# Kernel tuning notes

Hardware: AMD Instinct MI355X
Metric: run time of the kernel (lower is better)

The kernel has to match this reference:

```python
import jax, jax.numpy as jnp
import numpy as np


def setup_inputs() -> dict:
    key = jax.random.key(0)
    ks = jax.random.split(key, 8)
    B, T, C = 8, 2048, 1024
    X = jax.random.normal(ks[0], (B, T, C), dtype=jnp.float32)
    dX = jax.random.normal(ks[1], (B, T, C), dtype=jnp.float32)
    S_n = jnp.zeros((B, C), dtype=jnp.float32)
    att_mask = jnp.ones((B, T), dtype=jnp.int64)
    # parameters (torch init: randn(C,C)/C ; nn.Linear default uniform)
    W_Q = jax.random.normal(ks[2], (C, C), dtype=jnp.float32) / C
    W_K = jax.random.normal(ks[3], (C, C), dtype=jnp.float32) / C
    W_V = jax.random.normal(ks[4], (C, C), dtype=jnp.float32) / C
    bound = 1.0 / np.sqrt(C)
    W_hh = jax.random.uniform(ks[5], (C, C), minval=-bound, maxval=bound, dtype=jnp.float32)
    b_hh = jax.random.uniform(ks[6], (C,), minval=-bound, maxval=bound, dtype=jnp.float32)
    return {"X": X, "dX": dX, "S_n": S_n, "att_mask": att_mask,
            "W_Q": W_Q, "W_K": W_K, "W_V": W_V, "W_hh": W_hh, "b_hh": b_hh}


def reference(X, dX, S_n, att_mask, W_Q, W_K, W_V, W_hh, b_hh):
    B, T, C = X.shape
    # chunk_len is hard-coded to 1 in the source, so per-step:
    #   Q_t,K_t,V_t: [B,1,C]; c_t = Q_t @ K_t^T: [B,1,1]; A_t = c_t @ V_t.
    # These have no cross-timestep dependency -> precompute in parallel.
    Q = jax.nn.relu(jnp.einsum('btc,cd->btd', X, W_Q))
    K = jax.nn.relu(jnp.einsum('btc,cd->btd', X, W_K))
    V = jnp.einsum('btc,cd->btd', X, W_V)
    s = jnp.sum(Q * K, axis=-1, keepdims=True)        # [B,T,1]
    A = s * V                                          # [B,T,C]
    # A_factor = A_scale[chunk_len-1] = linspace(0,-1,ceil(T/2))[0] == 0.0
    A_scale = jnp.concatenate([jnp.linspace(0.0, -1.0, (T + 1) // 2),
                               jnp.linspace(-1.0, 0.0, T // 2)])
    A_factor = A_scale[0]

    def step(carry, A_t):
        h, prev_A = carry
        h_new = jnp.tanh(h @ W_hh.T + b_hh + A_t + prev_A * A_factor)
        return (h_new, A_t), h_new

    h0 = jnp.zeros((B, C), X.dtype)
    A_seq = jnp.swapaxes(A, 0, 1)                      # [T,B,C]
    _, H = jax.lax.scan(step, (h0, h0), A_seq)
    out = jnp.swapaxes(H, 0, 1)                        # [B,T,C]
    return out, S_n
```

## Files before the change

### kernel.cpp

```cpp
#include <hip/hip_runtime.h>
#include <hip/hip_bf16.h>

#define Bn 8
#define Tn 2048
#define Cn 1024

typedef __attribute__((ext_vector_type(8))) short short8;
typedef __attribute__((ext_vector_type(4))) float f32x4;

__device__ __forceinline__ unsigned short f2bf(float x) {
    union { float f; unsigned u; } v; v.f = x;
    return (unsigned short)((v.u + 0x7FFFu + ((v.u >> 16) & 1u)) >> 16);
}

__global__ __launch_bounds__(256) void transpose_cvt(const float* __restrict__ W,
                                                     unsigned short* __restrict__ WT) {
    __shared__ float tile[64][65];
    const int bx = blockIdx.x;
    const int tr = (bx >> 4) << 6;
    const int tc = (bx & 15) << 6;
    const int tid = threadIdx.x;
    const int r  = tid >> 2;
    const int c4 = (tid & 3) << 4;
#pragma unroll
    for (int i = 0; i < 4; ++i) {
        float4 v = *(const float4*)(W + (long)(tr + r) * Cn + tc + c4 + i * 4);
        tile[r][c4 + i * 4 + 0] = v.x;
        tile[r][c4 + i * 4 + 1] = v.y;
        tile[r][c4 + i * 4 + 2] = v.z;
        tile[r][c4 + i * 4 + 3] = v.w;
    }
    __syncthreads();
    short8 p0, p1;
#pragma unroll
    for (int i = 0; i < 8; ++i)  p0[i] = (short)f2bf(tile[c4 + i][r]);
#pragma unroll
    for (int i = 0; i < 8; ++i)  p1[i] = (short)f2bf(tile[c4 + 8 + i][r]);
    unsigned short* dst = WT + (long)(tc + r) * Cn + tr + c4;
    *(short8*)(dst)     = p0;
    *(short8*)(dst + 8) = p1;
}

__global__ __launch_bounds__(256, 1) void qkv_fused(const float* __restrict__ X,
                                                    const unsigned short* __restrict__ WqT,
                                                    const unsigned short* __restrict__ WkT,
                                                    const unsigned short* __restrict__ WvT,
                                                    float* __restrict__ Aout) {
    extern __shared__ char smem[];
    char* xs = smem;
    char* b0 = smem + 131072;
    char* b1 = smem + 147456;
    const int tid = threadIdx.x;
    const long row0 = (long)blockIdx.x * 64;

#pragma unroll 4
    for (int it = 0; it < 32; ++it) {
        int chunk = it * 256 + tid;
        int r  = chunk >> 7;
        int cc = chunk & 127;
        const float* src = X + (row0 + r) * Cn + cc * 8;
        float4 v0 = *(const float4*)src;
        float4 v1 = *(const float4*)(src + 4);
        short8 p;
        p[0] = (short)f2bf(v0.x); p[1] = (short)f2bf(v0.y);
        p[2] = (short)f2bf(v0.z); p[3] = (short)f2bf(v0.w);
        p[4] = (short)f2bf(v1.x); p[5] = (short)f2bf(v1.y);
        p[6] = (short)f2bf(v1.z); p[7] = (short)f2bf(v1.w);
        *(short8*)(xs + r * 2048 + ((cc * 16) ^ ((r & 7) << 4))) = p;
    }

    const int lane = tid & 63;
    const int wv   = tid >> 6;
    const int wm   = wv & 1;
    const int wn   = wv >> 1;
    const int m0   = wm * 32;
    const int l15  = lane & 15;
    const int lk   = lane >> 4;

    float s_part[2][4] = {};

    for (int nb = 0; nb < 8; ++nb) {
        const int n0 = nb * 128;
        f32x4 qa[2][4] = {};
        f32x4 ka[2][4] = {};
        for (int k0 = 0; k0 < 16; ++k0) {
            const int kk = k0 * 64;
            __syncthreads();
#pragma unroll
            for (int i = 0; i < 4; ++i) {
                int ch = i * 256 + tid;
                int n  = ch >> 3;
                int s  = ch & 7;
                int loff = n * 128 + ((s * 16) ^ ((n & 7) << 4));
                long goff = (long)(n0 + n) * Cn + kk + s * 8;
                *(short8*)(b0 + loff) = *(const short8*)(WqT + goff);
                *(short8*)(b1 + loff) = *(const short8*)(WkT + goff);
            }
            __syncthreads();
#pragma unroll
            for (int ki = 0; ki < 2; ++ki) {
                const int kb  = (kk + ki * 32 + lk * 8) * 2;
                const int r0  = m0 + l15, r1 = m0 + 16 + l15;
                short8 a0 = *(const short8*)(xs + r0 * 2048 + (kb ^ ((r0 & 7) << 4)));
                short8 a1 = *(const short8*)(xs + r1 * 2048 + (kb ^ ((r1 & 7) << 4)));
                const int bkb = (ki * 32 + lk * 8) * 2;
#pragma unroll
                for (int nf = 0; nf < 4; ++nf) {
                    int n = wn * 64 + nf * 16 + l15;
                    int boff = n * 128 + (bkb ^ ((n & 7) << 4));
                    short8 bq = *(const short8*)(b0 + boff);
                    qa[0][nf] = __builtin_amdgcn_mfma_f32_16x16x32_bf16(a0, bq, qa[0][nf], 0, 0, 0);
                    qa[1][nf] = __builtin_amdgcn_mfma_f32_16x16x32_bf16(a1, bq, qa[1][nf], 0, 0, 0);
                    short8 bk = *(const short8*)(b1 + boff);
                    ka[0][nf] = __builtin_amdgcn_mfma_f32_16x16x32_bf16(a0, bk, ka[0][nf], 0, 0, 0);
                    ka[1][nf] = __builtin_amdgcn_mfma_f32_16x16x32_bf16(a1, bk, ka[1][nf], 0, 0, 0);
                }
            }
        }
#pragma unroll
        for (int mf = 0; mf < 2; ++mf)
#pragma unroll
            for (int nf = 0; nf < 4; ++nf)
#pragma unroll
                for (int r = 0; r < 4; ++r) {
                    float q = fmaxf(qa[mf][nf][r], 0.f);
                    float k = fmaxf(ka[mf][nf][r], 0.f);
                    s_part[mf][r] += q * k;
                }
    }
#pragma unroll
    for (int mf = 0; mf < 2; ++mf)
#pragma unroll
        for (int r = 0; r < 4; ++r) {
            float v = s_part[mf][r];
            v += __shfl_xor(v, 1);
            v += __shfl_xor(v, 2);
            v += __shfl_xor(v, 4);
            v += __shfl_xor(v, 8);
            s_part[mf][r] = v;
        }

    {
        float* s_red = (float*)b1;
        if (l15 == 0) {
#pragma unroll
            for (int mf = 0; mf < 2; ++mf)
#pragma unroll
                for (int r = 0; r < 4; ++r)
                    s_red[wn * 64 + m0 + mf * 16 + lk * 4 + r] = s_part[mf][r];
        }
        __syncthreads();
#pragma unroll
        for (int mf = 0; mf < 2; ++mf)
#pragma unroll
            for (int r = 0; r < 4; ++r) {
                int row = m0 + mf * 16 + lk * 4 + r;
                s_part[mf][r] = s_red[row] + s_red[64 + row];
            }
        __syncthreads();
    }

    for (int nb = 0; nb < 8; ++nb) {
        const int n0 = nb * 128;
        f32x4 va[2][4] = {};
        for (int k0 = 0; k0 < 16; ++k0) {
            const int kk = k0 * 64;
            __syncthreads();
#pragma unroll
            for (int i = 0; i < 4; ++i) {
                int ch = i * 256 + tid;
                int n  = ch >> 3;
                int s  = ch & 7;
                *(short8*)(b0 + n * 128 + ((s * 16) ^ ((n & 7) << 4))) =
                    *(const short8*)(WvT + (long)(n0 + n) * Cn + kk + s * 8);
            }
            __syncthreads();
#pragma unroll
            for (int ki = 0; ki < 2; ++ki) {
                const int kb  = (kk + ki * 32 + lk * 8) * 2;
                const int r0  = m0 + l15, r1 = m0 + 16 + l15;
                short8 a0 = *(const short8*)(xs + r0 * 2048 + (kb ^ ((r0 & 7) << 4)));
                short8 a1 = *(const short8*)(xs + r1 * 2048 + (kb ^ ((r1 & 7) << 4)));
                const int bkb = (ki * 32 + lk * 8) * 2;
#pragma unroll
                for (int nf = 0; nf < 4; ++nf) {
                    int n = wn * 64 + nf * 16 + l15;
                    short8 bv = *(const short8*)(b0 + n * 128 + (bkb ^ ((n & 7) << 4)));
                    va[0][nf] = __builtin_amdgcn_mfma_f32_16x16x32_bf16(a0, bv, va[0][nf], 0, 0, 0);
                    va[1][nf] = __builtin_amdgcn_mfma_f32_16x16x32_bf16(a1, bv, va[1][nf], 0, 0, 0);
                }
            }
        }
#pragma unroll
        for (int mf = 0; mf < 2; ++mf)
#pragma unroll
            for (int nf = 0; nf < 4; ++nf)
#pragma unroll
                for (int r = 0; r < 4; ++r) {
                    long row = row0 + m0 + mf * 16 + lk * 4 + r;
                    int  col = n0 + wn * 64 + nf * 16 + l15;
                    Aout[row * Cn + col] = s_part[mf][r] * va[mf][nf][r];
                }
    }
}

__global__ __launch_bounds__(256, 2)
void recurrence(const float* __restrict__ A,
                const float* __restrict__ Whh,
                const float* __restrict__ bhh,
                unsigned long long* __restrict__ cbuf,
                float* __restrict__ out) {
    const int tid = threadIdx.x;
    const int b   = blockIdx.x & 7;
    const int sl  = blockIdx.x >> 3;
    const int j0  = sl * 32;
    const int j   = tid & 31;
    const int ch  = tid >> 5;

    __shared__ float sbuf[16000];
    float* h_lds = sbuf;
    float* part  = sbuf + 1024;

    float4 w[32];
    const float4* wp = (const float4*)(Whh + (long)(j0 + j) * Cn + ch * 128);
#pragma unroll
    for (int r = 0; r < 32; ++r) w[r] = wp[r];
#pragma unroll
    for (int r = 0; r < 32; ++r) {
        asm volatile("" : "+v"(w[r].x), "+v"(w[r].y), "+v"(w[r].z), "+v"(w[r].w));
    }

    const float bh = (tid < 32) ? bhh[j0 + tid] : 0.f;

    for (int t = 1; t <= Tn; ++t) {
        float a_val = 0.f;
        if (tid < 32) a_val = A[((long)b * Tn + (t - 1)) * Cn + j0 + tid];

        unsigned long long* src =
            cbuf + ((size_t)((t - 1) & 1) * Bn + b) * Cn + tid * 4;
        const unsigned expect = (unsigned)(t - 1);
        float v0 = 0.f, v1 = 0.f, v2 = 0.f, v3 = 0.f;
        unsigned pend = 0xF;
        do {
            if (pend & 1u) {
                unsigned long long p = __hip_atomic_load(src + 0, __ATOMIC_RELAXED,
                                                         __HIP_MEMORY_SCOPE_AGENT);
                if ((unsigned)(p >> 32) == expect) { v0 = __uint_as_float((unsigned)p); pend &= ~1u; }
            }
            if (pend & 2u) {
                unsigned long long p = __hip_atomic_load(src + 1, __ATOMIC_RELAXED,
                                                         __HIP_MEMORY_SCOPE_AGENT);
                if ((unsigned)(p >> 32) == expect) { v1 = __uint_as_float((unsigned)p); pend &= ~2u; }
            }
            if (pend & 4u) {
                unsigned long long p = __hip_atomic_load(src + 2, __ATOMIC_RELAXED,
                                                         __HIP_MEMORY_SCOPE_AGENT);
                if ((unsigned)(p >> 32) == expect) { v2 = __uint_as_float((unsigned)p); pend &= ~4u; }
            }
            if (pend & 8u) {
                unsigned long long p = __hip_atomic_load(src + 3, __ATOMIC_RELAXED,
                                                         __HIP_MEMORY_SCOPE_AGENT);
                if ((unsigned)(p >> 32) == expect) { v3 = __uint_as_float((unsigned)p); pend &= ~8u; }
            }
        } while (pend);
        *(float4*)(h_lds + tid * 4) = make_float4(v0, v1, v2, v3);
        __syncthreads();

        float ax = 0.f, ay = 0.f, az = 0.f, aw = 0.f;
#pragma unroll
        for (int r = 0; r < 32; ++r) {
            float4 h4 = *(const float4*)(h_lds + ch * 128 + r * 4);
            ax = fmaf(w[r].x, h4.x, ax);
            ay = fmaf(w[r].y, h4.y, ay);
            az = fmaf(w[r].z, h4.z, az);
            aw = fmaf(w[r].w, h4.w, aw);
        }
        part[ch * 32 + j] = (ax + ay) + (az + aw);
        __syncthreads();

        if (tid < 32) {
            float s = 0.f;
#pragma unroll
            for (int c = 0; c < 8; ++c) s += part[c * 32 + tid];
            float ht = tanhf(s + a_val + bh);
            out[((long)b * Tn + (t - 1)) * Cn + j0 + tid] = ht;
            unsigned long long pk =
                ((unsigned long long)(unsigned)t << 32) | (unsigned long long)__float_as_uint(ht);
            __hip_atomic_store(cbuf + ((size_t)(t & 1) * Bn + b) * Cn + j0 + tid, pk,
                               __ATOMIC_RELAXED, __HIP_MEMORY_SCOPE_AGENT);
        }
        __syncthreads();
    }
}

extern "C" void kernel_launch(void* const* d_in, const int* in_sizes, int n_in,
                              void* d_out, int out_size, void* d_ws, size_t ws_size,
                              hipStream_t stream) {
    const float* X   = (const float*)d_in[0];
    const float* S_n = (const float*)d_in[2];
    const float* W_Q = (const float*)d_in[4];
    const float* W_K = (const float*)d_in[5];
    const float* W_V = (const float*)d_in[6];
    const float* Whh = (const float*)d_in[7];
    const float* bhh = (const float*)d_in[8];
    float* out = (float*)d_out;

    char* ws = (char*)d_ws;
    float*              A     = (float*)ws;
    unsigned short*     WqT   = (unsigned short*)(ws + 67108864);
    unsigned short*     WkT   = WqT + 1024 * 1024;
    unsigned short*     WvT   = WkT + 1024 * 1024;
    unsigned long long* cbuf  = (unsigned long long*)(ws + 67108864 + 3 * 2097152);

    (void)hipFuncSetAttribute((const void*)qkv_fused,
                              hipFuncAttributeMaxDynamicSharedMemorySize, 163840);

    (void)hipMemsetAsync(cbuf, 0, 2 * Bn * Cn * sizeof(unsigned long long), stream);

    transpose_cvt<<<256, 256, 0, stream>>>(W_Q, WqT);
    transpose_cvt<<<256, 256, 0, stream>>>(W_K, WkT);
    transpose_cvt<<<256, 256, 0, stream>>>(W_V, WvT);

    qkv_fused<<<256, 256, 163840, stream>>>(X, WqT, WkT, WvT, A);

    recurrence<<<256, 256, 0, stream>>>(A, Whh, bhh, cbuf, out);

    (void)hipMemcpyAsync(out + (long)Bn * Tn * Cn, S_n, Bn * Cn * sizeof(float),
                         hipMemcpyDeviceToDevice, stream);
}
```

Measured before the change: 4.912 ms.

## Use wave shuffles for hidden-state broadcast and cut per-step block barriers

The recurrence step now spreads the polled hidden-state values with wavefront shuffles instead of staging them through LDS. That removes one LDS write/read round trip and one barrier per timestep. Partial sums are combined across half-waves with shfl_xor, and a double-buffered partial array lets the trailing __syncthreads be dropped. The polling loop keeps two sets of atomic loads in flight to hide latency, and the h store to cbuf is issued before the output write. The latency-bound serial loop loses barriers, but each step now runs 128 shuffles, and correctness depends on the double-buffer reasoning.

```diff
diff --git a/kernel.cpp b/kernel.cpp
--- a/kernel.cpp
+++ b/kernel.cpp
@@ -204,6 +204,8 @@
     }
 }
 
+#define LDW(i) __hip_atomic_load(src + (i), __ATOMIC_RELAXED, __HIP_MEMORY_SCOPE_AGENT)
+
 __global__ __launch_bounds__(256, 2)
 void recurrence(const float* __restrict__ A,
                 const float* __restrict__ Whh,
@@ -214,15 +216,14 @@
     const int b   = blockIdx.x & 7;
     const int sl  = blockIdx.x >> 3;
     const int j0  = sl * 32;
-    const int j   = tid & 31;
-    const int ch  = tid >> 5;
+    const int g   = tid >> 5;
+    const int l   = tid & 31;
 
     __shared__ float sbuf[16000];
-    float* h_lds = sbuf;
-    float* part  = sbuf + 1024;
+    float (*part2)[4][32] = (float (*)[4][32])sbuf;
 
     float4 w[32];
-    const float4* wp = (const float4*)(Whh + (long)(j0 + j) * Cn + ch * 128);
+    const float4* wp = (const float4*)(Whh + (long)(j0 + l) * Cn + g * 128);
 #pragma unroll
     for (int r = 0; r < 32; ++r) w[r] = wp[r];
 #pragma unroll
@@ -231,65 +232,61 @@
     }
 
     const float bh = (tid < 32) ? bhh[j0 + tid] : 0.f;
+    const int   sb = tid & 32;
 
     for (int t = 1; t <= Tn; ++t) {
         float a_val = 0.f;
         if (tid < 32) a_val = A[((long)b * Tn + (t - 1)) * Cn + j0 + tid];
 
         unsigned long long* src =
-            cbuf + ((size_t)((t - 1) & 1) * Bn + b) * Cn + tid * 4;
+            cbuf + ((size_t)((t - 1) & 1) * Bn + b) * Cn + g * 128 + l * 4;
         const unsigned expect = (unsigned)(t - 1);
         float v0 = 0.f, v1 = 0.f, v2 = 0.f, v3 = 0.f;
         unsigned pend = 0xF;
-        do {
-            if (pend & 1u) {
-                unsigned long long p = __hip_atomic_load(src + 0, __ATOMIC_RELAXED,
-                                                         __HIP_MEMORY_SCOPE_AGENT);
-                if ((unsigned)(p >> 32) == expect) { v0 = __uint_as_float((unsigned)p); pend &= ~1u; }
-            }
-            if (pend & 2u) {
-                unsigned long long p = __hip_atomic_load(src + 1, __ATOMIC_RELAXED,
-                                                         __HIP_MEMORY_SCOPE_AGENT);
-                if ((unsigned)(p >> 32) == expect) { v1 = __uint_as_float((unsigned)p); pend &= ~2u; }
-            }
-            if (pend & 4u) {
-                unsigned long long p = __hip_atomic_load(src + 2, __ATOMIC_RELAXED,
-                                                         __HIP_MEMORY_SCOPE_AGENT);
-                if ((unsigned)(p >> 32) == expect) { v2 = __uint_as_float((unsigned)p); pend &= ~4u; }
-            }
-            if (pend & 8u) {
-                unsigned long long p = __hip_atomic_load(src + 3, __ATOMIC_RELAXED,
-                                                         __HIP_MEMORY_SCOPE_AGENT);
-                if ((unsigned)(p >> 32) == expect) { v3 = __uint_as_float((unsigned)p); pend &= ~8u; }
-            }
-        } while (pend);
-        *(float4*)(h_lds + tid * 4) = make_float4(v0, v1, v2, v3);
+        unsigned long long a0 = LDW(0), a1 = LDW(1), a2 = LDW(2), a3 = LDW(3);
+        for (;;) {
+            unsigned long long c0 = LDW(0), c1 = LDW(1), c2 = LDW(2), c3 = LDW(3);
+            if ((pend & 1u) && (unsigned)(a0 >> 32) == expect) { v0 = __uint_as_float((unsigned)a0); pend &= ~1u; }
+            if ((pend & 2u) && (unsigned)(a1 >> 32) == expect) { v1 = __uint_as_float((unsigned)a1); pend &= ~2u; }
+            if ((pend & 4u) && (unsigned)(a2 >> 32) == expect) { v2 = __uint_as_float((unsigned)a2); pend &= ~4u; }
+            if ((pend & 8u) && (unsigned)(a3 >> 32) == expect) { v3 = __uint_as_float((unsigned)a3); pend &= ~8u; }
+            if (!pend) break;
+            a0 = LDW(0); a1 = LDW(1); a2 = LDW(2); a3 = LDW(3);
+            if ((pend & 1u) && (unsigned)(c0 >> 32) == expect) { v0 = __uint_as_float((unsigned)c0); pend &= ~1u; }
+            if ((pend & 2u) && (unsigned)(c1 >> 32) == expect) { v1 = __uint_as_float((unsigned)c1); pend &= ~2u; }
+            if ((pend & 4u) && (unsigned)(c2 >> 32) == expect) { v2 = __uint_as_float((unsigned)c2); pend &= ~4u; }
+            if ((pend & 8u) && (unsigned)(c3 >> 32) == expect) { v3 = __uint_as_float((unsigned)c3); pend &= ~8u; }
+            if (!pend) break;
+        }
+
+        float ax = 0.f, ay = 0.f, az = 0.f, aw = 0.f;
+#pragma unroll
+        for (int s = 0; s < 32; ++s) {
+            float h0 = __shfl(v0, sb + s, 64);
+            float h1 = __shfl(v1, sb + s, 64);
+            float h2 = __shfl(v2, sb + s, 64);
+            float h3 = __shfl(v3, sb + s, 64);
+            ax = fmaf(w[s].x, h0, ax);
+            ay = fmaf(w[s].y, h1, ay);
+            az = fmaf(w[s].z, h2, az);
+            aw = fmaf(w[s].w, h3, aw);
+        }
+        float pt = (ax + ay) + (az + aw);
+        pt += __shfl_xor(pt, 32, 64);
+
+        if ((tid & 63) < 32) part2[t & 1][tid >> 6][l] = pt;
         __syncthreads();
 
-        float ax = 0.f, ay = 0.f, az = 0.f, aw = 0.f;
-#pragma unroll
-        for (int r = 0; r < 32; ++r) {
-            float4 h4 = *(const float4*)(h_lds + ch * 128 + r * 4);
-            ax = fmaf(w[r].x, h4.x, ax);
-            ay = fmaf(w[r].y, h4.y, ay);
-            az = fmaf(w[r].z, h4.z, az);
-            aw = fmaf(w[r].w, h4.w, aw);
-        }
-        part[ch * 32 + j] = (ax + ay) + (az + aw);
-        __syncthreads();
-
         if (tid < 32) {
-            float s = 0.f;
-#pragma unroll
-            for (int c = 0; c < 8; ++c) s += part[c * 32 + tid];
+            float s = (part2[t & 1][0][tid] + part2[t & 1][1][tid]) +
+                      (part2[t & 1][2][tid] + part2[t & 1][3][tid]);
             float ht = tanhf(s + a_val + bh);
-            out[((long)b * Tn + (t - 1)) * Cn + j0 + tid] = ht;
             unsigned long long pk =
                 ((unsigned long long)(unsigned)t << 32) | (unsigned long long)__float_as_uint(ht);
             __hip_atomic_store(cbuf + ((size_t)(t & 1) * Bn + b) * Cn + j0 + tid, pk,
                                __ATOMIC_RELAXED, __HIP_MEMORY_SCOPE_AGENT);
-        }
-        __syncthreads();
+            out[((long)b * Tn + (t - 1)) * Cn + j0 + tid] = ht;
+        }
     }
 }
 
```

After: 13.44 ms. +173.7%, slower.
